# Kernel tuning notes

Hardware: AMD Instinct MI355X
Metric: run time of the kernel (lower is better)

## Reference

```python
import jax, jax.numpy as jnp
import numpy as np

H = 60.0  # self.h
C = jnp.array([10665991.0, 27000000.0, 7953253.0], dtype=jnp.float32)  # self.c (9e6*3 = 27e6)


def setup_inputs() -> dict:
    key = jax.random.key(0)
    k1, k2, k3 = jax.random.split(key, 3)
    B, T = 8192, 1024
    # room temperatures in Kelvin, strictly positive (model uses 1/x)
    x0 = 280.0 + 20.0 * jax.random.uniform(k1, (B, 3), dtype=jnp.float32)
    u = jax.random.uniform(k2, (B, T, 8), dtype=jnp.float32)
    # col 0: external temperature ~[250,300] K; cols 1..7: positive power/irradiation
    u = u.at[:, :, 0].set(250.0 + 50.0 * u[:, :, 0])
    u = u.at[:, :, 1:].multiply(1000.0)
    # 14 scalar log-conductance params: [l12, l23, le1..3, ls1..3, lh1..3, lc1..3]
    lam = 0.1 * jax.random.normal(k3, (14,), dtype=jnp.float32)
    return {"x0": x0, "u": u, "lam": lam}


def _forward(x0, u, lam):
    e = jnp.exp(lam)
    e12, e23 = e[0], e[1]
    ee, es, eh, ec = e[2:5], e[5:8], e[8:11], e[11:14]  # each [3]

    def step(x, ut):  # x: [B,3], ut: [B,8]
        inv = 1.0 / x
        d12 = inv[:, 0] - inv[:, 1]
        d23 = inv[:, 1] - inv[:, 2]
        # A @ x^T, with A's only nonzeros at (0,1),(1,0),(1,2),(2,1)
        Ax = jnp.stack([
            e12 * d12 * x[:, 1],
            -e12 * d12 * x[:, 0] + e23 * d23 * x[:, 2],
            -e23 * d23 * x[:, 1],
        ], axis=-1)  # [B,3]
        u0 = ut[:, 0:1]  # external temperature
        # B @ u_t: external exchange + solar + per-room heating (u2..4) + cooling (u5..7)
        Bu = (ee * (inv - 1.0 / u0) * u0
              + es * ut[:, 1:2]
              + eh * ut[:, 2:5]
              + ec * ut[:, 5:8])  # [B,3]
        x_new = x * jnp.exp(H * (Ax + Bu) / C)
        return x_new, x_new

    # loop runs for T-1 steps using u[:, t] for t = 0..T-2
    u_seq = jnp.swapaxes(u[:, :-1, :], 0, 1)  # [T-1, B, 8]
    _, xs = jax.lax.scan(step, x0, u_seq)
    preds_rest = jnp.swapaxes(xs, 0, 1)  # [B, T-1, 3]
    # rows where the NEXT step's external temp is ~0 are flagged with -1
    invalid = u[:, 1:, 0] < 1e-6  # [B, T-1]
    preds_rest = jnp.where(invalid[..., None], jnp.float32(-1.0), preds_rest)
    return jnp.concatenate([x0[:, None, :], preds_rest], axis=1)  # [B, T, 3]


def reference(x0, u, lam):
    return _forward(x0, u, lam)
```

## Files before the change

kernel.cpp:

```cpp
#include <hip/hip_runtime.h>


#if __has_builtin(__builtin_amdgcn_exp2f)
#define EXP2F(x) __builtin_amdgcn_exp2f(x)
#else
#define EXP2F(x) __expf((x) * 0.69314718056f)
#endif

namespace {
constexpr int T = 1024;
constexpr int NBLK = T / 8;
constexpr float LOG2E = 1.4426950408889634f;
}

__device__ __forceinline__ float bcast8(float v, int idx) {
    return __int_as_float(__builtin_amdgcn_ds_bpermute(idx, __float_as_int(v)));
}

__global__ __launch_bounds__(256, 1) void bm_fwd(
    const float* __restrict__ x0p,
    const float* __restrict__ up,
    const float* __restrict__ lamp,
    float* __restrict__ outp)
{
    const int tid   = blockIdx.x * 256 + threadIdx.x;
    const int chain = tid >> 3;
    const int phase = tid & 7;
    const int idx_base = (threadIdx.x & 56) << 2;

    float e[14];
#pragma unroll
    for (int i = 0; i < 14; ++i) e[i] = expf(lamp[i]);
    const float e12 = e[0], e23 = e[1];
    const float ee0 = e[2], ee1 = e[3], ee2 = e[4];
    const float es0 = e[5], es1 = e[6], es2 = e[7];
    const float eh0 = e[8], eh1 = e[9], eh2 = e[10];
    const float ec0 = e[11], ec1 = e[12], ec2 = e[13];

    const float hc0 = (60.0f / 10665991.0f) * LOG2E;
    const float hc1 = (60.0f / 27000000.0f) * LOG2E;
    const float hc2 = (60.0f / 7953253.0f) * LOG2E;

    float X0 = x0p[3 * chain + 0];
    float X1 = x0p[3 * chain + 1];
    float X2 = x0p[3 * chain + 2];

    const float4* __restrict__ ub = (const float4*)(up + (size_t)chain * (T * 8));
    float* __restrict__ ob = outp + (size_t)chain * (T * 3);

    float4 A0, A1, B0, B1;

    auto loadA = [&](int j) {
        const float4* s = ub + (size_t)(8 * j + phase) * 2;
        A0 = s[0]; A1 = s[1];
    };
    auto loadB = [&](int j) {
        const float4* s = ub + (size_t)(8 * j + phase) * 2;
        B0 = s[0]; B1 = s[1];
    };

    auto procblk = [&](const float4& r0, const float4& r1, int j, bool first) {
        const float u0 = r0.x;
        const float Pk0 = fmaf(ec0, r1.y, fmaf(eh0, r0.z, fmaf(es0, r0.y, -ee0)));
        const float Pk1 = fmaf(ec1, r1.z, fmaf(eh1, r0.w, fmaf(es1, r0.y, -ee1)));
        const float Pk2 = fmaf(ec2, r1.w, fmaf(eh2, r1.x, fmaf(es2, r0.y, -ee2)));

        float W[8], Q0[8], Q1[8], Q2[8];
#pragma unroll
        for (int i = 0; i < 8; ++i) {
            const int idx = idx_base + (i << 2);
            W[i]  = bcast8(u0, idx);
            Q0[i] = bcast8(Pk0, idx);
            Q1[i] = bcast8(Pk1, idx);
            Q2[i] = bcast8(Pk2, idx);
        }

        float O0 = 0.0f, O1 = 0.0f, O2 = 0.0f;
#pragma unroll
        for (int i = 0; i < 8; ++i) {
            const bool bad = (W[i] < 1e-6f) && !(first && i == 0);
            if (phase == i) {
                O0 = bad ? -1.0f : X0;
                O1 = bad ? -1.0f : X1;
                O2 = bad ? -1.0f : X2;
            }
            const float i0 = __builtin_amdgcn_rcpf(X0);
            const float i1 = __builtin_amdgcn_rcpf(X1);
            const float i2 = __builtin_amdgcn_rcpf(X2);
            const float t12 = e12 * (i0 - i1);
            const float t23 = e23 * (i1 - i2);
            const float b0 = fmaf(ee0, W[i] * i0, Q0[i]);
            const float b1 = fmaf(ee1, W[i] * i1, Q1[i]);
            const float b2 = fmaf(ee2, W[i] * i2, Q2[i]);
            const float z0 = fmaf(t12, X1, b0);
            const float z1 = fmaf(t23, X2, fmaf(-t12, X0, b1));
            const float z2 = fmaf(-t23, X1, b2);
            X0 *= EXP2F(hc0 * z0);
            X1 *= EXP2F(hc1 * z1);
            X2 *= EXP2F(hc2 * z2);
        }
        float* o = ob + (size_t)(8 * j + phase) * 3;
        o[0] = O0; o[1] = O1; o[2] = O2;
    };

    loadA(0);
    loadB(1);
    procblk(A0, A1, 0, true);
    for (int j = 1; j < NBLK - 1; j += 2) {
        loadA(j + 1);
        procblk(B0, B1, j, false);
        loadB(j + 2);
        procblk(A0, A1, j + 1, false);
    }
    procblk(B0, B1, NBLK - 1, false);
}

extern "C" void kernel_launch(void* const* d_in, const int* in_sizes, int n_in,
                              void* d_out, int out_size, void* d_ws, size_t ws_size,
                              hipStream_t stream) {
    const float* x0  = (const float*)d_in[0];
    const float* u   = (const float*)d_in[1];
    const float* lam = (const float*)d_in[2];
    float* out = (float*)d_out;

    const int B = in_sizes[0] / 3;
    const int threads = B * 8;
    dim3 grid(threads / 256), block(256);
    hipLaunchKernelGGL(bm_fwd, grid, block, 0, stream, x0, u, lam, out);
}
```

Measured before the change: 436.7 us.

## Broadcast per-step inputs via swizzled LDS instead of ds_bpermute, prefold constants

Replaces the 32 per-block ds_bpermute broadcasts with each lane writing six precomputed coefficients to a bank-swizzled LDS slot, which the chain's lanes then read back as vector loads. Folds the H/C*log2e scaling and the ee*u0 products into the per-lane precompute, so the serial recurrence runs fewer multiplies per step. Moves the invalid-row check to the owning lane after the loop. The LDS reuse is not synchronised, but it stays within a wavefront.

```diff
diff --git a/kernel.cpp b/kernel.cpp
--- a/kernel.cpp
+++ b/kernel.cpp
@@ -11,10 +11,7 @@
 constexpr int T = 1024;
 constexpr int NBLK = T / 8;
 constexpr float LOG2E = 1.4426950408889634f;
-}
-
-__device__ __forceinline__ float bcast8(float v, int idx) {
-    return __int_as_float(__builtin_amdgcn_ds_bpermute(idx, __float_as_int(v)));
+constexpr int CH_STRIDE = 68;
 }
 
 __global__ __launch_bounds__(256, 1) void bm_fwd(
@@ -23,23 +20,29 @@
     const float* __restrict__ lamp,
     float* __restrict__ outp)
 {
+    __shared__ float lds[32 * CH_STRIDE];
+
     const int tid   = blockIdx.x * 256 + threadIdx.x;
     const int chain = tid >> 3;
     const int phase = tid & 7;
-    const int idx_base = (threadIdx.x & 56) << 2;
+    const int g     = (threadIdx.x >> 3) & 7;
+    float* __restrict__ region = lds + (threadIdx.x >> 3) * CH_STRIDE;
+    float* __restrict__ wslot  = region + ((phase ^ g) << 3);
 
     float e[14];
 #pragma unroll
     for (int i = 0; i < 14; ++i) e[i] = expf(lamp[i]);
     const float e12 = e[0], e23 = e[1];
-    const float ee0 = e[2], ee1 = e[3], ee2 = e[4];
-    const float es0 = e[5], es1 = e[6], es2 = e[7];
-    const float eh0 = e[8], eh1 = e[9], eh2 = e[10];
-    const float ec0 = e[11], ec1 = e[12], ec2 = e[13];
 
     const float hc0 = (60.0f / 10665991.0f) * LOG2E;
     const float hc1 = (60.0f / 27000000.0f) * LOG2E;
     const float hc2 = (60.0f / 7953253.0f) * LOG2E;
+    const float F12_0 = hc0 * e12, F12_1 = hc1 * e12;
+    const float F23_1 = hc1 * e23, F23_2 = hc2 * e23;
+    const float hce0 = hc0 * e[2],  hce1 = hc1 * e[3],  hce2 = hc2 * e[4];
+    const float ss0  = hc0 * e[5],  ss1  = hc1 * e[6],  ss2  = hc2 * e[7];
+    const float sh0  = hc0 * e[8],  sh1  = hc1 * e[9],  sh2  = hc2 * e[10];
+    const float sc0  = hc0 * e[11], sc1  = hc1 * e[12], sc2  = hc2 * e[13];
 
     float X0 = x0p[3 * chain + 0];
     float X1 = x0p[3 * chain + 1];
@@ -48,71 +51,65 @@
     const float4* __restrict__ ub = (const float4*)(up + (size_t)chain * (T * 8));
     float* __restrict__ ob = outp + (size_t)chain * (T * 3);
 
-    float4 A0, A1, B0, B1;
+    auto body = [&](int j, float4& r0, float4& r1) {
+        const float my_u0 = r0.x;
+        const float E0 = hce0 * r0.x, E1 = hce1 * r0.x, E2 = hce2 * r0.x;
+        const float G0 = fmaf(sc0, r1.y, fmaf(sh0, r0.z, fmaf(ss0, r0.y, -hce0)));
+        const float G1 = fmaf(sc1, r1.z, fmaf(sh1, r0.w, fmaf(ss1, r0.y, -hce1)));
+        const float G2 = fmaf(sc2, r1.w, fmaf(sh2, r1.x, fmaf(ss2, r0.y, -hce2)));
+        *(float4*)wslot       = make_float4(E0, E1, E2, G0);
+        *(float2*)(wslot + 4) = make_float2(G1, G2);
 
-    auto loadA = [&](int j) {
-        const float4* s = ub + (size_t)(8 * j + phase) * 2;
-        A0 = s[0]; A1 = s[1];
-    };
-    auto loadB = [&](int j) {
-        const float4* s = ub + (size_t)(8 * j + phase) * 2;
-        B0 = s[0]; B1 = s[1];
-    };
+        {
+            const int jj = (j + 2 < NBLK) ? (j + 2) : (NBLK - 1);
+            const float4* s = ub + (size_t)(((jj << 3) + phase) * 2);
+            r0 = s[0]; r1 = s[1];
+        }
 
-    auto procblk = [&](const float4& r0, const float4& r1, int j, bool first) {
-        const float u0 = r0.x;
-        const float Pk0 = fmaf(ec0, r1.y, fmaf(eh0, r0.z, fmaf(es0, r0.y, -ee0)));
-        const float Pk1 = fmaf(ec1, r1.z, fmaf(eh1, r0.w, fmaf(es1, r0.y, -ee1)));
-        const float Pk2 = fmaf(ec2, r1.w, fmaf(eh2, r1.x, fmaf(es2, r0.y, -ee2)));
-
-        float W[8], Q0[8], Q1[8], Q2[8];
+        float4 bA[8]; float2 bB[8];
 #pragma unroll
         for (int i = 0; i < 8; ++i) {
-            const int idx = idx_base + (i << 2);
-            W[i]  = bcast8(u0, idx);
-            Q0[i] = bcast8(Pk0, idx);
-            Q1[i] = bcast8(Pk1, idx);
-            Q2[i] = bcast8(Pk2, idx);
+            float* p = region + ((i ^ g) << 3);
+            bA[i] = *(float4*)p;
+            bB[i] = *(float2*)(p + 4);
         }
 
         float O0 = 0.0f, O1 = 0.0f, O2 = 0.0f;
 #pragma unroll
         for (int i = 0; i < 8; ++i) {
-            const bool bad = (W[i] < 1e-6f) && !(first && i == 0);
-            if (phase == i) {
-                O0 = bad ? -1.0f : X0;
-                O1 = bad ? -1.0f : X1;
-                O2 = bad ? -1.0f : X2;
-            }
+            if (phase == i) { O0 = X0; O1 = X1; O2 = X2; }
             const float i0 = __builtin_amdgcn_rcpf(X0);
             const float i1 = __builtin_amdgcn_rcpf(X1);
             const float i2 = __builtin_amdgcn_rcpf(X2);
-            const float t12 = e12 * (i0 - i1);
-            const float t23 = e23 * (i1 - i2);
-            const float b0 = fmaf(ee0, W[i] * i0, Q0[i]);
-            const float b1 = fmaf(ee1, W[i] * i1, Q1[i]);
-            const float b2 = fmaf(ee2, W[i] * i2, Q2[i]);
-            const float z0 = fmaf(t12, X1, b0);
-            const float z1 = fmaf(t23, X2, fmaf(-t12, X0, b1));
-            const float z2 = fmaf(-t23, X1, b2);
-            X0 *= EXP2F(hc0 * z0);
-            X1 *= EXP2F(hc1 * z1);
-            X2 *= EXP2F(hc2 * z2);
+            const float d12 = i0 - i1, d23 = i1 - i2;
+            const float z0 = fmaf(F12_0 * d12, X1, fmaf(bA[i].x, i0, bA[i].w));
+            const float z1 = fmaf(F23_1 * d23, X2,
+                             fmaf(-(F12_1 * d12), X0, fmaf(bA[i].y, i1, bB[i].x)));
+            const float z2 = fmaf(-(F23_2 * d23), X1, fmaf(bA[i].z, i2, bB[i].y));
+            X0 *= EXP2F(z0);
+            X1 *= EXP2F(z1);
+            X2 *= EXP2F(z2);
         }
-        float* o = ob + (size_t)(8 * j + phase) * 3;
-        o[0] = O0; o[1] = O1; o[2] = O2;
+
+        const bool bad = (my_u0 < 1e-6f) && !((j == 0) & (phase == 0));
+        float3 o;
+        o.x = bad ? -1.0f : O0;
+        o.y = bad ? -1.0f : O1;
+        o.z = bad ? -1.0f : O2;
+        *(float3*)(ob + (size_t)((j << 3) + phase) * 3) = o;
     };
 
-    loadA(0);
-    loadB(1);
-    procblk(A0, A1, 0, true);
-    for (int j = 1; j < NBLK - 1; j += 2) {
-        loadA(j + 1);
-        procblk(B0, B1, j, false);
-        loadB(j + 2);
-        procblk(A0, A1, j + 1, false);
+    float4 a0, a1, b0, b1;
+    {
+        const float4* s = ub + (size_t)(phase * 2);
+        a0 = s[0]; a1 = s[1];
+        const float4* t = ub + (size_t)((8 + phase) * 2);
+        b0 = t[0]; b1 = t[1];
     }
-    procblk(B0, B1, NBLK - 1, false);
+    for (int j = 0; j < NBLK; j += 2) {
+        body(j,     a0, a1);
+        body(j + 1, b0, b1);
+    }
 }
 
 extern "C" void kernel_launch(void* const* d_in, const int* in_sizes, int n_in,
```

New measurement: 413.9 us. -5.2%, faster.
